# Kernel optimization log

Hardware: AMD Instinct MI355X
Metric: run time of the kernel (lower is better)

## Reference

```python
import jax, jax.numpy as jnp
import numpy as np


def setup_inputs() -> dict:
    key = jax.random.key(0)
    k1, k2 = jax.random.split(key)
    B, L, D, R = 32, 512, 1024, 128
    batch = jax.random.normal(k1, (B, L, D), dtype=jnp.float32)
    # nn.init.uniform_(proj, -0.05, 0.05)
    proj = jax.random.uniform(k2, (D, R), dtype=jnp.float32, minval=-0.05, maxval=0.05)
    return {"batch": batch, "proj": proj}


def reference(batch, proj):
    # transformed: (B, L, R)
    t = jnp.matmul(batch, proj)
    # Squared L2 all-pairs distance via ||a||^2 + ||b||^2 - 2 a.b
    # (same math as sum((t_i - t_j)^2, -1), avoids the O(B*L*L*R) intermediate)
    sq_norms = jnp.sum(t * t, axis=-1)                      # (B, L)
    cross = jnp.einsum("bir,bjr->bij", t, t)               # (B, L, L)
    d = sq_norms[:, :, None] + sq_norms[:, None, :] - 2.0 * cross
    return jnp.maximum(d, 0.0)  # clamp tiny negative numerical noise
```

## Files before the change

### kernel.cpp

```cpp
#include <hip/hip_runtime.h>
#include <hip/hip_bf16.h>


typedef __attribute__((ext_vector_type(8))) short bf16x8;
typedef __attribute__((ext_vector_type(4))) float f32x4;

__device__ __forceinline__ unsigned short f2bf(float f) {
    unsigned u = __float_as_uint(f);
    unsigned r = (u + 0x7fffu + ((u >> 16) & 1u)) >> 16;
    return (unsigned short)r;
}
__device__ __forceinline__ float bf2f(unsigned short h) {
    return __uint_as_float(((unsigned)h) << 16);
}
__device__ __forceinline__ bf16x8 pack8(float4 x, float4 y) {
    bf16x8 r;
    r[0] = (short)f2bf(x.x); r[1] = (short)f2bf(x.y);
    r[2] = (short)f2bf(x.z); r[3] = (short)f2bf(x.w);
    r[4] = (short)f2bf(y.x); r[5] = (short)f2bf(y.y);
    r[6] = (short)f2bf(y.z); r[7] = (short)f2bf(y.w);
    return r;
}

__global__ __launch_bounds__(256) void transpose_proj(const float* __restrict__ proj,
                                                      unsigned short* __restrict__ projT) {
    __shared__ unsigned short TsT[128][40];
    const int k0 = blockIdx.x * 32;
    const int t = threadIdx.x;
    const int kl = t >> 3;
    const int seg = t & 7;
    const float* src = proj + (k0 + kl) * 128 + seg * 16;
#pragma unroll
    for (int i = 0; i < 4; ++i) {
        float4 v = *(const float4*)(src + 4 * i);
        int c = seg * 16 + 4 * i;
        TsT[c + 0][kl] = f2bf(v.x);
        TsT[c + 1][kl] = f2bf(v.y);
        TsT[c + 2][kl] = f2bf(v.z);
        TsT[c + 3][kl] = f2bf(v.w);
    }
    __syncthreads();
    const int r = t >> 1, h = t & 1;
#pragma unroll
    for (int i = 0; i < 2; ++i) {
        *(uint4*)(projT + r * 1024 + k0 + h * 16 + 8 * i) =
            *(const uint4*)&TsT[r][h * 16 + 8 * i];
    }
}

__global__ __launch_bounds__(256) void gemm_t(const float* __restrict__ batch,
                                              const unsigned short* __restrict__ projT,
                                              unsigned short* __restrict__ tOut,
                                              float* __restrict__ sqn) {
    __shared__ float sqpart[2][2][16];

    const int t = threadIdx.x;
    const int wave = t >> 6, lane = t & 63;
    const int wm = wave >> 1, wn = wave & 1;
    const int quad = lane >> 4, l15 = lane & 15;
    const int m0 = blockIdx.x * 32;

    f32x4 acc[4] = {};

    const float* aptr = batch + (m0 + wm * 16 + l15) * 1024 + quad * 8;
    const unsigned short* bptr[4];
#pragma unroll
    for (int fn = 0; fn < 4; ++fn)
        bptr[fn] = projT + (wn * 64 + fn * 16 + l15) * 1024 + quad * 8;

#pragma unroll 2
    for (int kk = 0; kk < 1024; kk += 64) {
        float4 a0 = *(const float4*)(aptr + kk);
        float4 a1 = *(const float4*)(aptr + kk + 4);
        float4 a2 = *(const float4*)(aptr + kk + 32);
        float4 a3 = *(const float4*)(aptr + kk + 36);
        bf16x8 b0[4], b1[4];
#pragma unroll
        for (int fn = 0; fn < 4; ++fn) {
            b0[fn] = *(const bf16x8*)(bptr[fn] + kk);
            b1[fn] = *(const bf16x8*)(bptr[fn] + kk + 32);
        }
        bf16x8 af0 = pack8(a0, a1);
        bf16x8 af1 = pack8(a2, a3);
#pragma unroll
        for (int fn = 0; fn < 4; ++fn)
            acc[fn] = __builtin_amdgcn_mfma_f32_16x16x32_bf16(af0, b0[fn], acc[fn], 0, 0, 0);
#pragma unroll
        for (int fn = 0; fn < 4; ++fn)
            acc[fn] = __builtin_amdgcn_mfma_f32_16x16x32_bf16(af1, b1[fn], acc[fn], 0, 0, 0);
    }

    float p[4] = {0.f, 0.f, 0.f, 0.f};
#pragma unroll
    for (int fn = 0; fn < 4; ++fn) {
        int col = wn * 64 + fn * 16 + l15;
#pragma unroll
        for (int reg = 0; reg < 4; ++reg) {
            int row = m0 + wm * 16 + quad * 4 + reg;
            unsigned short hb = f2bf(acc[fn][reg]);
            tOut[row * 128 + col] = hb;
            float fv = bf2f(hb);
            p[reg] += fv * fv;
        }
    }
#pragma unroll
    for (int off = 1; off < 16; off <<= 1) {
#pragma unroll
        for (int reg = 0; reg < 4; ++reg) p[reg] += __shfl_xor(p[reg], off);
    }
    if (l15 == 0) {
#pragma unroll
        for (int reg = 0; reg < 4; ++reg) sqpart[wm][wn][quad * 4 + reg] = p[reg];
    }
    __syncthreads();
    if (t < 32) {
        int wmi = t >> 4, ridx = t & 15;
        sqn[m0 + wmi * 16 + ridx] = sqpart[wmi][0][ridx] + sqpart[wmi][1][ridx];
    }
}

__global__ __launch_bounds__(256) void dist_k(const unsigned short* __restrict__ tMat,
                                              const float* __restrict__ sqn,
                                              float* __restrict__ out) {
    const int bx = blockIdx.x;
    const int b = bx >> 4, it = (bx >> 2) & 3, jt = bx & 3;
    const int i0 = it * 128, j0 = jt * 128;
    const int t = threadIdx.x;
    const int wave = t >> 6, lane = t & 63;
    const int quad = lane >> 4, l15 = lane & 15;

    const unsigned short* abase = tMat + (b * 512 + j0 + wave * 32 + l15) * 128 + quad * 8;
    uint4 araw[2][4];
#pragma unroll
    for (int fm = 0; fm < 2; ++fm)
#pragma unroll
        for (int ksi = 0; ksi < 4; ++ksi)
            araw[fm][ksi] = *(const uint4*)(abase + fm * 16 * 128 + ksi * 32);

    const float* sqb = sqn + b * 512;
    float sqj_[2][4], sqi_[8];
#pragma unroll
    for (int fm = 0; fm < 2; ++fm)
#pragma unroll
        for (int reg = 0; reg < 4; ++reg)
            sqj_[fm][reg] = sqb[j0 + wave * 32 + fm * 16 + quad * 4 + reg];
#pragma unroll
    for (int fn = 0; fn < 8; ++fn)
        sqi_[fn] = sqb[i0 + fn * 16 + l15];

    const unsigned short* bbase = tMat + (b * 512 + i0 + l15) * 128 + quad * 8;

    f32x4 acc[2][8] = {};
#pragma unroll
    for (int ksi = 0; ksi < 4; ++ksi) {
        bf16x8 bfr[8];
#pragma unroll
        for (int fn = 0; fn < 8; ++fn)
            bfr[fn] = *(const bf16x8*)(bbase + fn * 16 * 128 + ksi * 32);
#pragma unroll
        for (int fm = 0; fm < 2; ++fm) {
            bf16x8 af = *(const bf16x8*)&araw[fm][ksi];
#pragma unroll
            for (int fn = 0; fn < 8; ++fn)
                acc[fm][fn] = __builtin_amdgcn_mfma_f32_16x16x32_bf16(af, bfr[fn], acc[fm][fn], 0, 0, 0);
        }
    }

    float* obase = out + (size_t)b * 512 * 512;
#pragma unroll
    for (int fn = 0; fn < 8; ++fn) {
        const int i = i0 + fn * 16 + l15;
        float* orow = obase + (size_t)i * 512 + j0;
        const float si = sqi_[fn];
#pragma unroll
        for (int fm = 0; fm < 2; ++fm) {
            float4 v;
            v.x = fmaxf(si + sqj_[fm][0] - 2.0f * acc[fm][fn][0], 0.0f);
            v.y = fmaxf(si + sqj_[fm][1] - 2.0f * acc[fm][fn][1], 0.0f);
            v.z = fmaxf(si + sqj_[fm][2] - 2.0f * acc[fm][fn][2], 0.0f);
            v.w = fmaxf(si + sqj_[fm][3] - 2.0f * acc[fm][fn][3], 0.0f);
            *(float4*)(orow + wave * 32 + fm * 16 + quad * 4) = v;
        }
    }
}

extern "C" void kernel_launch(void* const* d_in, const int* in_sizes, int n_in,
                              void* d_out, int out_size, void* d_ws, size_t ws_size,
                              hipStream_t stream) {
    (void)in_sizes; (void)n_in; (void)out_size; (void)ws_size;
    const float* batch = (const float*)d_in[0];
    const float* proj  = (const float*)d_in[1];
    float* out = (float*)d_out;

    unsigned short* projT = (unsigned short*)d_ws;
    unsigned short* tMat  = projT + 128 * 1024;
    float* sqn = (float*)(tMat + 16384 * 128);

    hipLaunchKernelGGL(transpose_proj, dim3(32),  dim3(256), 0, stream, proj, projT);
    hipLaunchKernelGGL(gemm_t,         dim3(512), dim3(256), 0, stream, batch, projT, tMat, sqn);
    hipLaunchKernelGGL(dist_k,         dim3(512), dim3(256), 0, stream, tMat, sqn, out);
}
```

Measured before the change: 148.5 us.

## Stage GEMM and distance operands through LDS via async global-to-LDS loads

Replaces per-wave direct global loads in both the projection GEMM and the distance kernel with global_load_lds copies into shared memory. The GEMM double-buffers 64-wide K slices so loads for the next slice overlap compute on the current one. The distance kernel shares each block's operand tiles via LDS instead of every wave re-reading them. This raises LDS usage per block, which may reduce occupancy, and relies on barriers to cover async load completion.

```diff
diff --git a/kernel.cpp b/kernel.cpp
--- a/kernel.cpp
+++ b/kernel.cpp
@@ -4,6 +4,15 @@
 
 typedef __attribute__((ext_vector_type(8))) short bf16x8;
 typedef __attribute__((ext_vector_type(4))) float f32x4;
+
+typedef __attribute__((address_space(3))) unsigned lds_u;
+typedef __attribute__((address_space(1))) const unsigned gbl_u;
+
+__device__ __forceinline__ void async16(void* lds, const void* g) {
+    __builtin_amdgcn_global_load_lds((gbl_u*)(unsigned long long)g,
+                                     (lds_u*)(unsigned)(unsigned long long)lds,
+                                     16, 0, 0);
+}
 
 __device__ __forceinline__ unsigned short f2bf(float f) {
     unsigned u = __float_as_uint(f);
@@ -52,6 +61,7 @@
                                               const unsigned short* __restrict__ projT,
                                               unsigned short* __restrict__ tOut,
                                               float* __restrict__ sqn) {
+    __shared__ unsigned char Ls[2][24 * 1024];
     __shared__ float sqpart[2][2][16];
 
     const int t = threadIdx.x;
@@ -60,34 +70,51 @@
     const int quad = lane >> 4, l15 = lane & 15;
     const int m0 = blockIdx.x * 32;
 
+    const float* aSrc = batch + (m0 + (wave >> 1) * 16 + l15) * 1024
+                      + (wave & 1) * 32 + quad * 8;
+    const unsigned short* bSrc[4];
+#pragma unroll
+    for (int c = 0; c < 4; ++c) {
+        int bi = c * 4 + wave;
+        bSrc[c] = projT + ((bi >> 3) * 64 + ((bi >> 1) & 3) * 16 + l15) * 1024
+                + (bi & 1) * 32 + quad * 8;
+    }
+
     f32x4 acc[4] = {};
 
-    const float* aptr = batch + (m0 + wm * 16 + l15) * 1024 + quad * 8;
-    const unsigned short* bptr[4];
-#pragma unroll
-    for (int fn = 0; fn < 4; ++fn)
-        bptr[fn] = projT + (wn * 64 + fn * 16 + l15) * 1024 + quad * 8;
-
-#pragma unroll 2
-    for (int kk = 0; kk < 1024; kk += 64) {
-        float4 a0 = *(const float4*)(aptr + kk);
-        float4 a1 = *(const float4*)(aptr + kk + 4);
-        float4 a2 = *(const float4*)(aptr + kk + 32);
-        float4 a3 = *(const float4*)(aptr + kk + 36);
-        bf16x8 b0[4], b1[4];
+    auto stage = [&](int buf, int kk) {
+        unsigned char* base = &Ls[buf][0];
+        async16(base + (wave * 2 + 0) * 1024 + lane * 16, aSrc + kk);
+        async16(base + (wave * 2 + 1) * 1024 + lane * 16, aSrc + kk + 4);
+#pragma unroll
+        for (int c = 0; c < 4; ++c) {
+            int bi = c * 4 + wave;
+            async16(base + 8192 + bi * 1024 + lane * 16, bSrc[c] + kk);
+        }
+    };
+
+    stage(0, 0);
+#pragma unroll
+    for (int s = 0; s < 16; ++s) {
+        __syncthreads();
+        if (s < 15) stage((s + 1) & 1, (s + 1) * 64);
+        const unsigned char* base = &Ls[s & 1][0];
+        bf16x8 af[2];
+#pragma unroll
+        for (int h = 0; h < 2; ++h) {
+            float4 f0 = *(const float4*)(base + ((wm * 2 + h) * 2 + 0) * 1024 + lane * 16);
+            float4 f1 = *(const float4*)(base + ((wm * 2 + h) * 2 + 1) * 1024 + lane * 16);
+            af[h] = pack8(f0, f1);
+        }
 #pragma unroll
         for (int fn = 0; fn < 4; ++fn) {
-            b0[fn] = *(const bf16x8*)(bptr[fn] + kk);
-            b1[fn] = *(const bf16x8*)(bptr[fn] + kk + 32);
-        }
-        bf16x8 af0 = pack8(a0, a1);
-        bf16x8 af1 = pack8(a2, a3);
-#pragma unroll
-        for (int fn = 0; fn < 4; ++fn)
-            acc[fn] = __builtin_amdgcn_mfma_f32_16x16x32_bf16(af0, b0[fn], acc[fn], 0, 0, 0);
-#pragma unroll
-        for (int fn = 0; fn < 4; ++fn)
-            acc[fn] = __builtin_amdgcn_mfma_f32_16x16x32_bf16(af1, b1[fn], acc[fn], 0, 0, 0);
+#pragma unroll
+            for (int h = 0; h < 2; ++h) {
+                int bi = wn * 8 + fn * 2 + h;
+                bf16x8 bfr = *(const bf16x8*)(base + 8192 + bi * 1024 + lane * 16);
+                acc[fn] = __builtin_amdgcn_mfma_f32_16x16x32_bf16(af[h], bfr, acc[fn], 0, 0, 0);
+            }
+        }
     }
 
     float p[4] = {0.f, 0.f, 0.f, 0.f};
@@ -122,6 +149,8 @@
 __global__ __launch_bounds__(256) void dist_k(const unsigned short* __restrict__ tMat,
                                               const float* __restrict__ sqn,
                                               float* __restrict__ out) {
+    __shared__ unsigned char Ls[64 * 1024];
+
     const int bx = blockIdx.x;
     const int b = bx >> 4, it = (bx >> 2) & 3, jt = bx & 3;
     const int i0 = it * 128, j0 = jt * 128;
@@ -129,13 +158,19 @@
     const int wave = t >> 6, lane = t & 63;
     const int quad = lane >> 4, l15 = lane & 15;
 
-    const unsigned short* abase = tMat + (b * 512 + j0 + wave * 32 + l15) * 128 + quad * 8;
-    uint4 araw[2][4];
-#pragma unroll
-    for (int fm = 0; fm < 2; ++fm)
-#pragma unroll
-        for (int ksi = 0; ksi < 4; ++ksi)
-            araw[fm][ksi] = *(const uint4*)(abase + fm * 16 * 128 + ksi * 32);
+    const unsigned short* aS = tMat + (b * 512 + j0 + wave * 32 + l15) * 128 + quad * 8;
+#pragma unroll
+    for (int c = 0; c < 8; ++c)
+        async16(&Ls[(wave * 8 + c) * 1024 + lane * 16],
+                aS + (c >> 2) * 16 * 128 + (c & 3) * 32);
+
+    const unsigned short* bS = tMat + (b * 512 + i0 + l15) * 128 + quad * 8;
+#pragma unroll
+    for (int c = 0; c < 8; ++c) {
+        int bi = c * 4 + wave;
+        async16(&Ls[32768 + bi * 1024 + lane * 16],
+                bS + (bi >> 2) * 16 * 128 + (bi & 3) * 32);
+    }
 
     const float* sqb = sqn + b * 512;
     float sqj_[2][4], sqi_[8];
@@ -148,21 +183,21 @@
     for (int fn = 0; fn < 8; ++fn)
         sqi_[fn] = sqb[i0 + fn * 16 + l15];
 
-    const unsigned short* bbase = tMat + (b * 512 + i0 + l15) * 128 + quad * 8;
+    __syncthreads();
 
     f32x4 acc[2][8] = {};
 #pragma unroll
     for (int ksi = 0; ksi < 4; ++ksi) {
-        bf16x8 bfr[8];
-#pragma unroll
-        for (int fn = 0; fn < 8; ++fn)
-            bfr[fn] = *(const bf16x8*)(bbase + fn * 16 * 128 + ksi * 32);
-#pragma unroll
-        for (int fm = 0; fm < 2; ++fm) {
-            bf16x8 af = *(const bf16x8*)&araw[fm][ksi];
-#pragma unroll
-            for (int fn = 0; fn < 8; ++fn)
-                acc[fm][fn] = __builtin_amdgcn_mfma_f32_16x16x32_bf16(af, bfr[fn], acc[fm][fn], 0, 0, 0);
+        bf16x8 af[2];
+#pragma unroll
+        for (int fm = 0; fm < 2; ++fm)
+            af[fm] = *(const bf16x8*)&Ls[(wave * 8 + fm * 4 + ksi) * 1024 + lane * 16];
+#pragma unroll
+        for (int fn = 0; fn < 8; ++fn) {
+            bf16x8 bfr = *(const bf16x8*)&Ls[32768 + (fn * 4 + ksi) * 1024 + lane * 16];
+#pragma unroll
+            for (int fm = 0; fm < 2; ++fm)
+                acc[fm][fn] = __builtin_amdgcn_mfma_f32_16x16x32_bf16(af[fm], bfr, acc[fm][fn], 0, 0, 0);
         }
     }
 
```

Measured after the change: 128.4 us. -13.5%, faster.
